# Kernel tuning notes

Measured on AMD Instinct MI355X. Metric: run time of the kernel, lower is better.

## Reference

```python
import jax, jax.numpy as jnp
import numpy as np

B, S, H, NH = 2, 2048, 2048, 16
HD = H // NH
SCALE = 1.0 / np.sqrt(HD).astype(np.float32)


def setup_inputs() -> dict:
    key = jax.random.key(0)
    ks = jax.random.split(key, 10)
    std = 1.0 / np.sqrt(H)
    return {
        "x": jax.random.normal(ks[0], (B, S, H), dtype=jnp.float32),
        "attention_mask": jnp.zeros((B, 1, 1, S), dtype=jnp.float32),
        "Wq": jax.random.normal(ks[1], (H, H), dtype=jnp.float32) * std,
        "bq": jnp.zeros((H,), dtype=jnp.float32),
        "Wk": jax.random.normal(ks[2], (H, H), dtype=jnp.float32) * std,
        "bk": jnp.zeros((H,), dtype=jnp.float32),
        "Wv": jax.random.normal(ks[3], (H, H), dtype=jnp.float32) * std,
        "bv": jnp.zeros((H,), dtype=jnp.float32),
        "Wo": jax.random.normal(ks[4], (H, H), dtype=jnp.float32) * std,
        "bo": jnp.zeros((H,), dtype=jnp.float32),
    }


def _heads(t):
    # [B,S,H] -> [B,NH,S,HD]
    return t.reshape(B, S, NH, HD).transpose(0, 2, 1, 3)


def reference(x, attention_mask, Wq, bq, Wk, bk, Wv, bv, Wo, bo):
    q = _heads(x @ Wq.T + bq)
    k = _heads(x @ Wk.T + bk)
    v = _heads(x @ Wv.T + bv)
    scores = jnp.einsum("bhqd,bhkd->bhqk", q, k) * SCALE + attention_mask
    probs = jax.nn.softmax(scores, axis=-1)
    ctx = jnp.einsum("bhqk,bhkd->bhqd", probs, v)
    ctx = ctx.transpose(0, 2, 1, 3).reshape(B, S, H)
    return ctx @ Wo.T + bo
```

## Files before the change

### kernel.cpp

```cpp
#include <hip/hip_runtime.h>
#include <cstdint>
#include <cstddef>

#define B_   2
#define S_   2048
#define H_   2048
#define NH_  16
#define HD_  128
#define MM_  (B_ * S_)
#define K_   H_
#define SCALE_F 0.08838834764831845f
#define LOG2E_F 1.4426950408889634f
#define QSCALE_F (SCALE_F * LOG2E_F)

typedef __bf16 bf16_t;
typedef __attribute__((ext_vector_type(8))) __bf16 bf16x8;
typedef __attribute__((ext_vector_type(4))) float  f32x4;
typedef __attribute__((ext_vector_type(4))) float  floatx4;

static __device__ __forceinline__ f32x4 mfma_16x16x32(bf16x8 a, bf16x8 b, f32x4 c) {
  return __builtin_amdgcn_mfma_f32_16x16x32_bf16(a, b, c, 0, 0, 0);
}

static __device__ __forceinline__ void gl2lds16(const bf16_t* g, bf16_t* l) {
  __builtin_amdgcn_global_load_lds(
      (const __attribute__((address_space(1))) void*)g,
      (__attribute__((address_space(3))) void*)l, 16, 0, 0);
}

static __device__ __forceinline__ float exp2_hw(float x) {
  float r;
  asm("v_exp_f32 %0, %1" : "=v"(r) : "v"(x));
  return r;
}

__global__ void cvt6_f32_bf16(const float* __restrict__ x,
                              const float* __restrict__ w0, const float* __restrict__ w1,
                              const float* __restrict__ w2, const float* __restrict__ w3,
                              bf16_t* xo, bf16_t* o0, bf16_t* o1, bf16_t* o2, bf16_t* o3,
                              int n8) {
  const int yy = blockIdx.y;
  const float* in;
  bf16_t* out;
  if (yy == 0)      { in = x;                      out = xo; }
  else if (yy == 1) { in = x + (size_t)H_ * H_;    out = xo + (size_t)H_ * H_; }
  else if (yy == 2) { in = w0; out = o0; }
  else if (yy == 3) { in = w1; out = o1; }
  else if (yy == 4) { in = w2; out = o2; }
  else              { in = w3; out = o3; }
  int i = blockIdx.x * blockDim.x + threadIdx.x;
  const int stride = gridDim.x * blockDim.x;
  for (; i < n8; i += stride) {
    const floatx4* p = (const floatx4*)(in + (size_t)i * 8);
    floatx4 a = p[0], b = p[1];
    bf16x8 o;
    o[0] = (bf16_t)a.x; o[1] = (bf16_t)a.y; o[2] = (bf16_t)a.z; o[3] = (bf16_t)a.w;
    o[4] = (bf16_t)b.x; o[5] = (bf16_t)b.y; o[6] = (bf16_t)b.z; o[7] = (bf16_t)b.w;
    *(bf16x8*)(out + (size_t)i * 8) = o;
  }
}

template <int MODE, int NCOLS>
__global__ __launch_bounds__(256) void gemm_bt(
    const bf16_t* __restrict__ A,
    const bf16_t* __restrict__ W0, const bf16_t* __restrict__ W1, const bf16_t* __restrict__ W2,
    const float* __restrict__ bias0, const float* __restrict__ bias1, const float* __restrict__ bias2,
    bf16_t* __restrict__ dq, bf16_t* __restrict__ dk, bf16_t* __restrict__ dv,
    float* __restrict__ outf)
{
  __shared__ __align__(16) bf16_t Ash[128 * 32];
  __shared__ __align__(16) bf16_t Bsh[128 * 32];

  const int t = threadIdx.x;
  const int lane = t & 63;
  const int wid  = t >> 6;
  const int wm = wid >> 1, wn = wid & 1;

  const int lin = blockIdx.x;
  const int xcd = lin & 7;
  const int loc = lin >> 3;
  const int sr  = loc >> 5;
  const int l   = loc & 31;
  const int r_  = xcd * (NCOLS / 8) + sr;
  const int tm  = (r_ & 3) * 8 + (l & 7);
  const int nc  = (r_ >> 2) * 4 + (l >> 3);
  const int bm  = tm * 128;

  int bn;
  int wsel = 0;
  const bf16_t* Bw;
  const float*  bias;
  bf16_t* dsth = nullptr;
  if constexpr (MODE == 0) {
    wsel = nc >> 4;
    bn   = (nc & 15) * 128;
    Bw   = (wsel == 0) ? W0 : ((wsel == 1) ? W1 : W2);
    bias = (wsel == 0) ? bias0 : ((wsel == 1) ? bias1 : bias2);
    dsth = (wsel == 0) ? dq : ((wsel == 1) ? dk : dv);
  } else {
    bn = nc * 128;
    Bw = W0; bias = bias0;
  }

  const bf16_t* gA = A  + (size_t)(bm + (t >> 2)) * K_ + (t & 3) * 8;
  const bf16_t* gB = Bw + (size_t)(bn + (t >> 2)) * K_ + (t & 3) * 8;
  bf16_t* lA = Ash + wid * 512;
  bf16_t* lB = Bsh + wid * 512;

  f32x4 acc[4][4] = {};

  #pragma unroll 1
  for (int k0 = 0; k0 < K_; k0 += 32) {
    gl2lds16(gA + k0,                    lA);
    gl2lds16(gA + k0 + (size_t)64 * K_,  lA + 2048);
    gl2lds16(gB + k0,                    lB);
    gl2lds16(gB + k0 + (size_t)64 * K_,  lB + 2048);
    __syncthreads();

    bf16x8 af[4], bfr[4];
    #pragma unroll
    for (int i = 0; i < 4; ++i) {
      af[i]  = *(const bf16x8*)&Ash[(wm * 64 + i * 16 + (lane & 15)) * 32 + (lane >> 4) * 8];
      bfr[i] = *(const bf16x8*)&Bsh[(wn * 64 + i * 16 + (lane & 15)) * 32 + (lane >> 4) * 8];
    }
    __builtin_amdgcn_s_setprio(1);
    #pragma unroll
    for (int i = 0; i < 4; ++i)
      #pragma unroll
      for (int j = 0; j < 4; ++j)
        acc[i][j] = mfma_16x16x32(af[i], bfr[j], acc[i][j]);
    __builtin_amdgcn_s_setprio(0);
    __syncthreads();
  }

  const int row0 = bm + wm * 64 + (lane >> 4) * 4;
  const int col0 = bn + wn * 64 + (lane & 15);
  #pragma unroll
  for (int j = 0; j < 4; ++j) {
    const int col = col0 + j * 16;
    const float bv = bias[col];
    #pragma unroll
    for (int i = 0; i < 4; ++i) {
      #pragma unroll
      for (int r = 0; r < 4; ++r) {
        const int row = row0 + i * 16 + r;
        float v = acc[i][j][r] + bv;
        if constexpr (MODE == 0) {
          const int ss = row & (S_ - 1);
          const int dd = col & (HD_ - 1);
          const size_t bh = (size_t)((row >> 11) * NH_ + (col >> 7));
          if (wsel == 0) v *= QSCALE_F;
          size_t idx;
          if (wsel == 2) {
            const size_t t1 = bh * 32 + (ss >> 6);
            const size_t t2 = t1 * 8 + (dd >> 4);
            const size_t t3 = t2 * 2 + ((ss >> 5) & 1);
            const size_t ln = (size_t)((dd & 15) | (((ss >> 3) & 3) << 4));
            idx = (t3 * 64 + ln) * 8 + (size_t)(ss & 7);
          } else {
            const size_t t1 = bh * 128 + (ss >> 4);
            const size_t t2 = t1 * 4 + (dd >> 5);
            const size_t ln = (size_t)((ss & 15) | (((dd >> 3) & 3) << 4));
            idx = (t2 * 64 + ln) * 8 + (size_t)(dd & 7);
          }
          dsth[idx] = (bf16_t)v;
        } else {
          outf[(size_t)row * H_ + col] = v;
        }
      }
    }
  }
}

#define KVB 64
#define NT_ (S_ / KVB)
#define TILE_E 8192

__global__ __launch_bounds__(256, 4) void attn_kernel(
    const bf16_t* __restrict__ Qf, const bf16_t* __restrict__ Kf,
    const bf16_t* __restrict__ Vf, const float* __restrict__ mask,
    bf16_t* __restrict__ ctx)
{
  __shared__ __align__(16) bf16_t Klds[TILE_E];
  __shared__ __align__(16) bf16_t Vlds[TILE_E];
  __shared__ __align__(16) bf16_t Plds[4][16 * KVB];

  const int t = threadIdx.x;
  const int lane = t & 63;
  const int wid  = t >> 6;

  const int orig = blockIdx.x;
  const int wg = (orig & 7) * 128 + (orig >> 3);
  const int qt = wg & 31;
  const int bh = wg >> 5;
  const int b  = bh >> 4;
  const int h  = bh & 15;
  const int q0 = qt * 64 + wid * 16;

  const bf16_t* Kh0 = Kf + (size_t)bh * (NT_ * TILE_E);
  const bf16_t* Vh0 = Vf + (size_t)bh * (NT_ * TILE_E);
  const float*  mg  = mask + (size_t)b * S_;

  const bf16_t* Qt = Qf + (((size_t)bh * 128 + (q0 >> 4)) * 4) * 512;
  bf16x8 qf[4];
  #pragma unroll
  for (int ks = 0; ks < 4; ++ks)
    qf[ks] = *(const bf16x8*)&Qt[(ks * 64 + lane) * 8];

  f32x4 acc[8] = {};
  float m_run[4], l_run[4];
  #pragma unroll
  for (int r = 0; r < 4; ++r) { m_run[r] = -INFINITY; l_run[r] = 0.0f; }

  char* Pw = (char*)&Plds[wid][0];

  auto stage = [&](int it) {
    const bf16_t* Ksrc = Kh0 + (size_t)it * TILE_E;
    const bf16_t* Vsrc = Vh0 + (size_t)it * TILE_E;
    #pragma unroll
    for (int i = 0; i < 4; ++i) {
      const int base = (i * 256 + wid * 64) * 8;
      gl2lds16(Ksrc + base + lane * 8, &Klds[base]);
      gl2lds16(Vsrc + base + lane * 8, &Vlds[base]);
    }
  };

  #pragma unroll 1
  for (int it = 0; it < NT_; ++it) {
    stage(it);
    __syncthreads();

    f32x4 sacc[4] = {};
    #pragma unroll
    for (int ns = 0; ns < 4; ++ns) {
      #pragma unroll
      for (int ks = 0; ks < 4; ++ks) {
        const bf16x8 kf = *(const bf16x8*)&Klds[((ns * 4 + ks) * 64 + lane) * 8];
        __builtin_amdgcn_s_setprio(1);
        sacc[ns] = mfma_16x16x32(qf[ks], kf, sacc[ns]);
        __builtin_amdgcn_s_setprio(0);
      }
    }

    const int kv0 = it * KVB;
    float msk[4];
    #pragma unroll
    for (int ns = 0; ns < 4; ++ns)
      msk[ns] = mg[kv0 + ns * 16 + (lane & 15)] * LOG2E_F;

    float sv[4][4], tmax[4];
    #pragma unroll
    for (int r = 0; r < 4; ++r) tmax[r] = -INFINITY;
    #pragma unroll
    for (int ns = 0; ns < 4; ++ns)
      #pragma unroll
      for (int r = 0; r < 4; ++r) {
        sv[ns][r] = sacc[ns][r] + msk[ns];
        tmax[r] = fmaxf(tmax[r], sv[ns][r]);
      }
    #pragma unroll
    for (int off = 1; off < 16; off <<= 1)
      #pragma unroll
      for (int r = 0; r < 4; ++r)
        tmax[r] = fmaxf(tmax[r], __shfl_xor(tmax[r], off));

    bool small = true;
    #pragma unroll
    for (int r = 0; r < 4; ++r)
      small = small && (tmax[r] <= m_run[r] + 8.0f);
    if (!__all(small)) {
      float scl[4];
      #pragma unroll
      for (int r = 0; r < 4; ++r) {
        const float mnew = fmaxf(m_run[r], tmax[r]);
        scl[r] = exp2_hw(m_run[r] - mnew);
        m_run[r] = mnew;
        l_run[r] *= scl[r];
      }
      #pragma unroll
      for (int ds = 0; ds < 8; ++ds)
        #pragma unroll
        for (int r = 0; r < 4; ++r)
          acc[ds][r] *= scl[r];
    }

    float rsum[4] = {};
    #pragma unroll
    for (int ns = 0; ns < 4; ++ns)
      #pragma unroll
      for (int r = 0; r < 4; ++r) {
        const float p = exp2_hw(sv[ns][r] - m_run[r]);
        rsum[r] += p;
        const int qq = (lane >> 4) * 4 + r;
        const int pb = (qq << 7) + ((((ns << 5) | ((lane & 15) << 1))) ^ ((qq & 7) << 4));
        *(bf16_t*)(Pw + pb) = (bf16_t)p;
      }

    bf16x8 pf[2];
    #pragma unroll
    for (int k2 = 0; k2 < 2; ++k2) {
      const int qq = lane & 15;
      const int pb = (qq << 7) + (((k2 << 6) | ((lane >> 4) << 4)) ^ ((qq & 7) << 4));
      pf[k2] = *(const bf16x8*)(Pw + pb);
    }

    #pragma unroll
    for (int ds = 0; ds < 8; ++ds) {
      const bf16x8 vf0 = *(const bf16x8*)&Vlds[((ds * 2 + 0) * 64 + lane) * 8];
      const bf16x8 vf1 = *(const bf16x8*)&Vlds[((ds * 2 + 1) * 64 + lane) * 8];
      __builtin_amdgcn_s_setprio(1);
      acc[ds] = mfma_16x16x32(pf[0], vf0, acc[ds]);
      acc[ds] = mfma_16x16x32(pf[1], vf1, acc[ds]);
      __builtin_amdgcn_s_setprio(0);
    }

    #pragma unroll
    for (int off = 1; off < 16; off <<= 1)
      #pragma unroll
      for (int r = 0; r < 4; ++r)
        rsum[r] += __shfl_xor(rsum[r], off);
    #pragma unroll
    for (int r = 0; r < 4; ++r)
      l_run[r] += rsum[r];

    __syncthreads();
  }

  #pragma unroll
  for (int ds = 0; ds < 8; ++ds)
    #pragma unroll
    for (int r = 0; r < 4; ++r) {
      const int q = q0 + (lane >> 4) * 4 + r;
      const int d = ds * 16 + (lane & 15);
      ctx[((size_t)(b * S_ + q)) * H_ + h * HD_ + d] =
          (bf16_t)(acc[ds][r] / l_run[r]);
    }
}

extern "C" void kernel_launch(void* const* d_in, const int* in_sizes, int n_in,
                              void* d_out, int out_size, void* d_ws, size_t ws_size,
                              hipStream_t stream) {
  (void)in_sizes; (void)n_in; (void)out_size; (void)ws_size;
  const float* x    = (const float*)d_in[0];
  const float* mask = (const float*)d_in[1];
  const float* Wq   = (const float*)d_in[2];
  const float* bq   = (const float*)d_in[3];
  const float* Wk   = (const float*)d_in[4];
  const float* bk   = (const float*)d_in[5];
  const float* Wv   = (const float*)d_in[6];
  const float* bv   = (const float*)d_in[7];
  const float* Wo   = (const float*)d_in[8];
  const float* bo   = (const float*)d_in[9];
  float* out = (float*)d_out;

  const size_t nX = (size_t)MM_ * H_;
  const size_t nW = (size_t)H_ * H_;

  bf16_t* xbf = (bf16_t*)d_ws;
  bf16_t* wqb = xbf + nX;
  bf16_t* wkb = wqb + nW;
  bf16_t* wvb = wkb + nW;
  bf16_t* wob = wvb + nW;
  bf16_t* qf  = wob + nW;
  bf16_t* kf  = qf + nX;
  bf16_t* vf  = kf + nX;
  bf16_t* cxb = vf + nX;

  cvt6_f32_bf16<<<dim3(512, 6), 256, 0, stream>>>(
      x, Wq, Wk, Wv, Wo, xbf, wqb, wkb, wvb, wob, (int)(nW / 8));

  gemm_bt<0, 48><<<32 * 48, 256, 0, stream>>>(
      xbf, wqb, wkb, wvb, bq, bk, bv, qf, kf, vf, nullptr);

  attn_kernel<<<1024, 256, 0, stream>>>(qf, kf, vf, mask, cxb);

  gemm_bt<1, 16><<<32 * 16, 256, 0, stream>>>(
      cxb, wob, nullptr, nullptr, bo, nullptr, nullptr, nullptr, nullptr, nullptr, out);
}
```

Before: 348.6 us.

## Use two waves of 32 query rows each with transposed MFMA in attention

The attention block now runs 2 waves of 128 threads instead of 4, and each wave owns 32 query rows (two 16-row halves), so every K/V fragment read from LDS feeds two MFMAs. The MFMA operands are swapped so the score tile comes out transposed: each lane holds one query row and the row max and sum need only two cross-lane shuffles instead of four. P is written as packed bf16x4 in MFMA-fragment order, the mask is loaded as float4 before the barrier, and the output is stored as bf16x4. The trade-off is more registers per wave and fewer waves per block, which may lower occupancy and latency hiding.

```diff
diff --git a/kernel.cpp b/kernel.cpp
--- a/kernel.cpp
+++ b/kernel.cpp
@@ -15,6 +15,7 @@
 
 typedef __bf16 bf16_t;
 typedef __attribute__((ext_vector_type(8))) __bf16 bf16x8;
+typedef __attribute__((ext_vector_type(4))) __bf16 bf16x4;
 typedef __attribute__((ext_vector_type(4))) float  f32x4;
 typedef __attribute__((ext_vector_type(4))) float  floatx4;
 
@@ -176,18 +177,19 @@
 #define NT_ (S_ / KVB)
 #define TILE_E 8192
 
-__global__ __launch_bounds__(256, 4) void attn_kernel(
+__global__ __launch_bounds__(128, 2) void attn_kernel(
     const bf16_t* __restrict__ Qf, const bf16_t* __restrict__ Kf,
     const bf16_t* __restrict__ Vf, const float* __restrict__ mask,
     bf16_t* __restrict__ ctx)
 {
   __shared__ __align__(16) bf16_t Klds[TILE_E];
   __shared__ __align__(16) bf16_t Vlds[TILE_E];
-  __shared__ __align__(16) bf16_t Plds[4][16 * KVB];
+  __shared__ __align__(16) bf16_t Plds[2][2048];
 
   const int t = threadIdx.x;
   const int lane = t & 63;
   const int wid  = t >> 6;
+  const int g    = lane >> 4;
 
   const int orig = blockIdx.x;
   const int wg = (orig & 7) * 128 + (orig >> 3);
@@ -195,22 +197,23 @@
   const int bh = wg >> 5;
   const int b  = bh >> 4;
   const int h  = bh & 15;
-  const int q0 = qt * 64 + wid * 16;
+  const int q0 = qt * 64 + wid * 32;
 
   const bf16_t* Kh0 = Kf + (size_t)bh * (NT_ * TILE_E);
   const bf16_t* Vh0 = Vf + (size_t)bh * (NT_ * TILE_E);
   const float*  mg  = mask + (size_t)b * S_;
 
   const bf16_t* Qt = Qf + (((size_t)bh * 128 + (q0 >> 4)) * 4) * 512;
-  bf16x8 qf[4];
+  bf16x8 qf[2][4];
   #pragma unroll
-  for (int ks = 0; ks < 4; ++ks)
-    qf[ks] = *(const bf16x8*)&Qt[(ks * 64 + lane) * 8];
-
-  f32x4 acc[8] = {};
-  float m_run[4], l_run[4];
-  #pragma unroll
-  for (int r = 0; r < 4; ++r) { m_run[r] = -INFINITY; l_run[r] = 0.0f; }
+  for (int mh = 0; mh < 2; ++mh)
+    #pragma unroll
+    for (int ks = 0; ks < 4; ++ks)
+      qf[mh][ks] = *(const bf16x8*)&Qt[((mh * 4 + ks) * 64 + lane) * 8];
+
+  f32x4 acc[2][8] = {};
+  float m_run[2] = {-INFINITY, -INFINITY};
+  float l_run[2] = {0.0f, 0.0f};
 
   char* Pw = (char*)&Plds[wid][0];
 
@@ -218,8 +221,8 @@
     const bf16_t* Ksrc = Kh0 + (size_t)it * TILE_E;
     const bf16_t* Vsrc = Vh0 + (size_t)it * TILE_E;
     #pragma unroll
-    for (int i = 0; i < 4; ++i) {
-      const int base = (i * 256 + wid * 64) * 8;
+    for (int i = 0; i < 8; ++i) {
+      const int base = (i * 128 + wid * 64) * 8;
       gl2lds16(Ksrc + base + lane * 8, &Klds[base]);
       gl2lds16(Vsrc + base + lane * 8, &Vlds[base]);
     }
@@ -228,113 +231,121 @@
   #pragma unroll 1
   for (int it = 0; it < NT_; ++it) {
     stage(it);
+
+    const int kv0 = it * KVB;
+    floatx4 mv[4];
+    #pragma unroll
+    for (int ns = 0; ns < 4; ++ns)
+      mv[ns] = *(const floatx4*)&mg[kv0 + ns * 16 + g * 4];
+
     __syncthreads();
 
-    f32x4 sacc[4] = {};
+    f32x4 sacc[2][4] = {};
     #pragma unroll
     for (int ns = 0; ns < 4; ++ns) {
       #pragma unroll
       for (int ks = 0; ks < 4; ++ks) {
         const bf16x8 kf = *(const bf16x8*)&Klds[((ns * 4 + ks) * 64 + lane) * 8];
         __builtin_amdgcn_s_setprio(1);
-        sacc[ns] = mfma_16x16x32(qf[ks], kf, sacc[ns]);
+        sacc[0][ns] = mfma_16x16x32(kf, qf[0][ks], sacc[0][ns]);
+        sacc[1][ns] = mfma_16x16x32(kf, qf[1][ks], sacc[1][ns]);
         __builtin_amdgcn_s_setprio(0);
       }
     }
 
-    const int kv0 = it * KVB;
-    float msk[4];
-    #pragma unroll
-    for (int ns = 0; ns < 4; ++ns)
-      msk[ns] = mg[kv0 + ns * 16 + (lane & 15)] * LOG2E_F;
-
-    float sv[4][4], tmax[4];
-    #pragma unroll
-    for (int r = 0; r < 4; ++r) tmax[r] = -INFINITY;
-    #pragma unroll
-    for (int ns = 0; ns < 4; ++ns)
-      #pragma unroll
-      for (int r = 0; r < 4; ++r) {
-        sv[ns][r] = sacc[ns][r] + msk[ns];
-        tmax[r] = fmaxf(tmax[r], sv[ns][r]);
-      }
-    #pragma unroll
-    for (int off = 1; off < 16; off <<= 1)
-      #pragma unroll
-      for (int r = 0; r < 4; ++r)
-        tmax[r] = fmaxf(tmax[r], __shfl_xor(tmax[r], off));
-
-    bool small = true;
-    #pragma unroll
-    for (int r = 0; r < 4; ++r)
-      small = small && (tmax[r] <= m_run[r] + 8.0f);
+    float tmax[2];
+    #pragma unroll
+    for (int mh = 0; mh < 2; ++mh) {
+      float tm = -INFINITY;
+      #pragma unroll
+      for (int ns = 0; ns < 4; ++ns)
+        #pragma unroll
+        for (int r = 0; r < 4; ++r) {
+          sacc[mh][ns][r] += mv[ns][r];
+          tm = fmaxf(tm, sacc[mh][ns][r]);
+        }
+      tm = fmaxf(tm, __shfl_xor(tm, 16));
+      tm = fmaxf(tm, __shfl_xor(tm, 32));
+      tmax[mh] = tm;
+    }
+
+    const bool small = (tmax[0] <= m_run[0] + 8.0f) && (tmax[1] <= m_run[1] + 8.0f);
     if (!__all(small)) {
-      float scl[4];
-      #pragma unroll
-      for (int r = 0; r < 4; ++r) {
-        const float mnew = fmaxf(m_run[r], tmax[r]);
-        scl[r] = exp2_hw(m_run[r] - mnew);
-        m_run[r] = mnew;
-        l_run[r] *= scl[r];
-      }
-      #pragma unroll
-      for (int ds = 0; ds < 8; ++ds)
+      #pragma unroll
+      for (int mh = 0; mh < 2; ++mh) {
+        const float mnew = fmaxf(m_run[mh], tmax[mh]);
+        const float scl  = exp2_hw(m_run[mh] - mnew);
+        m_run[mh] = mnew;
+        l_run[mh] *= scl;
         #pragma unroll
-        for (int r = 0; r < 4; ++r)
-          acc[ds][r] *= scl[r];
-    }
-
-    float rsum[4] = {};
-    #pragma unroll
-    for (int ns = 0; ns < 4; ++ns)
-      #pragma unroll
-      for (int r = 0; r < 4; ++r) {
-        const float p = exp2_hw(sv[ns][r] - m_run[r]);
-        rsum[r] += p;
-        const int qq = (lane >> 4) * 4 + r;
-        const int pb = (qq << 7) + ((((ns << 5) | ((lane & 15) << 1))) ^ ((qq & 7) << 4));
-        *(bf16_t*)(Pw + pb) = (bf16_t)p;
-      }
-
-    bf16x8 pf[2];
-    #pragma unroll
-    for (int k2 = 0; k2 < 2; ++k2) {
-      const int qq = lane & 15;
-      const int pb = (qq << 7) + (((k2 << 6) | ((lane >> 4) << 4)) ^ ((qq & 7) << 4));
-      pf[k2] = *(const bf16x8*)(Pw + pb);
-    }
+        for (int ds = 0; ds < 8; ++ds)
+          #pragma unroll
+          for (int r = 0; r < 4; ++r)
+            acc[mh][ds][r] *= scl;
+      }
+    }
+
+    float rs[2] = {0.0f, 0.0f};
+    #pragma unroll
+    for (int mh = 0; mh < 2; ++mh) {
+      #pragma unroll
+      for (int ns = 0; ns < 4; ++ns) {
+        bf16x4 pk;
+        #pragma unroll
+        for (int r = 0; r < 4; ++r) {
+          const float p = exp2_hw(sacc[mh][ns][r] - m_run[mh]);
+          rs[mh] += p;
+          pk[r] = (bf16_t)p;
+        }
+        const int L = (lane & 15) | ((((ns & 1) << 1) | (g >> 1)) << 4);
+        const int byte = mh * 2048 + ((ns >> 1) << 10) + L * 16 + (g & 1) * 8;
+        *(bf16x4*)(Pw + byte) = pk;
+      }
+    }
+
+    bf16x8 pf[2][2];
+    #pragma unroll
+    for (int mh = 0; mh < 2; ++mh)
+      #pragma unroll
+      for (int ks2 = 0; ks2 < 2; ++ks2)
+        pf[mh][ks2] = *(const bf16x8*)(Pw + mh * 2048 + ks2 * 1024 + lane * 16);
 
     #pragma unroll
     for (int ds = 0; ds < 8; ++ds) {
       const bf16x8 vf0 = *(const bf16x8*)&Vlds[((ds * 2 + 0) * 64 + lane) * 8];
       const bf16x8 vf1 = *(const bf16x8*)&Vlds[((ds * 2 + 1) * 64 + lane) * 8];
       __builtin_amdgcn_s_setprio(1);
-      acc[ds] = mfma_16x16x32(pf[0], vf0, acc[ds]);
-      acc[ds] = mfma_16x16x32(pf[1], vf1, acc[ds]);
+      #pragma unroll
+      for (int mh = 0; mh < 2; ++mh) {
+        acc[mh][ds] = mfma_16x16x32(vf0, pf[mh][0], acc[mh][ds]);
+        acc[mh][ds] = mfma_16x16x32(vf1, pf[mh][1], acc[mh][ds]);
+      }
       __builtin_amdgcn_s_setprio(0);
     }
 
     #pragma unroll
-    for (int off = 1; off < 16; off <<= 1)
+    for (int mh = 0; mh < 2; ++mh) {
+      rs[mh] += __shfl_xor(rs[mh], 16);
+      rs[mh] += __shfl_xor(rs[mh], 32);
+      l_run[mh] += rs[mh];
+    }
+
+    __syncthreads();
+  }
+
+  #pragma unroll
+  for (int mh = 0; mh < 2; ++mh) {
+    const int q = q0 + mh * 16 + (lane & 15);
+    const float inv = 1.0f / l_run[mh];
+    #pragma unroll
+    for (int ds = 0; ds < 8; ++ds) {
+      bf16x4 o;
       #pragma unroll
       for (int r = 0; r < 4; ++r)
-        rsum[r] += __shfl_xor(rsum[r], off);
-    #pragma unroll
-    for (int r = 0; r < 4; ++r)
-      l_run[r] += rsum[r];
-
-    __syncthreads();
-  }
-
-  #pragma unroll
-  for (int ds = 0; ds < 8; ++ds)
-    #pragma unroll
-    for (int r = 0; r < 4; ++r) {
-      const int q = q0 + (lane >> 4) * 4 + r;
-      const int d = ds * 16 + (lane & 15);
-      ctx[((size_t)(b * S_ + q)) * H_ + h * HD_ + d] =
-          (bf16_t)(acc[ds][r] / l_run[r]);
-    }
+        o[r] = (bf16_t)(acc[mh][ds][r] * inv);
+      *(bf16x4*)&ctx[((size_t)(b * S_ + q)) * H_ + h * HD_ + ds * 16 + g * 4] = o;
+    }
+  }
 }
 
 extern "C" void kernel_launch(void* const* d_in, const int* in_sizes, int n_in,
@@ -372,7 +383,7 @@
   gemm_bt<0, 48><<<32 * 48, 256, 0, stream>>>(
       xbf, wqb, wkb, wvb, bq, bk, bv, qf, kf, vf, nullptr);
 
-  attn_kernel<<<1024, 256, 0, stream>>>(qf, kf, vf, mask, cxb);
+  attn_kernel<<<1024, 128, 0, stream>>>(qf, kf, vf, mask, cxb);
 
   gemm_bt<1, 16><<<32 * 16, 256, 0, stream>>>(
       cxb, wob, nullptr, nullptr, bo, nullptr, nullptr, nullptr, nullptr, nullptr, out);
```

Measured after the change: 308.9 us. -11.4%, faster.
